# Kernel optimization log

Measured on AMD Instinct MI355X. Metric: run time of the kernel, lower is better.

## Reference

```python
import jax, jax.numpy as jnp
import numpy as np
import math

B, S, F_IN = 8, 1024, 32
D, H, L, NCLS = 512, 8, 6, 3
DFF = 4 * D
DK = D // H
EPS = 1e-5


def make_pe(max_len, d_model):
    pos = jnp.arange(max_len, dtype=jnp.float32)[:, None]
    div = jnp.exp(jnp.arange(0, d_model, 2, dtype=jnp.float32) * (-math.log(10000.0) / d_model))
    pe = jnp.zeros((max_len, d_model), dtype=jnp.float32)
    pe = pe.at[:, 0::2].set(jnp.sin(pos * div))
    pe = pe.at[:, 1::2].set(jnp.cos(pos * div))
    return pe  # [max_len, D]


def layernorm(x, g, b):
    m = jnp.mean(x, -1, keepdims=True)
    v = jnp.mean((x - m) ** 2, -1, keepdims=True)
    return (x - m) * jax.lax.rsqrt(v + EPS) * g + b


def setup_inputs() -> dict:
    key = jax.random.key(0)
    ks = iter(jax.random.split(key, 40))

    def w(shape, scale=None):
        k = next(ks)
        s = scale if scale is not None else 1.0 / math.sqrt(shape[0])
        return jax.random.normal(k, shape, dtype=jnp.float32) * s

    inp = {
        'x': jax.random.normal(next(ks), (B, S, F_IN), dtype=jnp.float32),
        'pe': make_pe(S, D),
        'emb_w': w((F_IN, D)), 'emb_b': jnp.zeros((D,), jnp.float32),
        'Wq': w((L, D, D)), 'bq': jnp.zeros((L, D), jnp.float32),
        'Wk': w((L, D, D)), 'bk': jnp.zeros((L, D), jnp.float32),
        'Wv': w((L, D, D)), 'bv': jnp.zeros((L, D), jnp.float32),
        'Wo': w((L, D, D)), 'bo': jnp.zeros((L, D), jnp.float32),
        'ln1_g': jnp.ones((L, D), jnp.float32), 'ln1_b': jnp.zeros((L, D), jnp.float32),
        'ln2_g': jnp.ones((L, D), jnp.float32), 'ln2_b': jnp.zeros((L, D), jnp.float32),
        'W1': w((L, D, DFF)), 'b1': jnp.zeros((L, DFF), jnp.float32),
        'W2': w((L, DFF, D)), 'b2': jnp.zeros((L, D), jnp.float32),
        'fc1_w': w((D, 256)), 'fc1_b': jnp.zeros((256,), jnp.float32),
        'fc2_w': w((256, 128)), 'fc2_b': jnp.zeros((128,), jnp.float32),
        'fc3_w': w((128, NCLS)), 'fc3_b': jnp.zeros((NCLS,), jnp.float32),
    }
    return inp


def reference(x, pe, emb_w, emb_b, Wq, bq, Wk, bk, Wv, bv, Wo, bo,
              ln1_g, ln1_b, ln2_g, ln2_b, W1, b1, W2, b2,
              fc1_w, fc1_b, fc2_w, fc2_b, fc3_w, fc3_b):
    scale = math.sqrt(DK)
    h = x @ emb_w + emb_b                      # [B,S,D]
    h = h + pe[None, :S, :]                    # positional encoding
    for l in range(L):
        # multi-head self-attention (full O(S^2) scores, as in source)
        q = (h @ Wq[l] + bq[l]).reshape(B, S, H, DK).transpose(0, 2, 1, 3)
        k = (h @ Wk[l] + bk[l]).reshape(B, S, H, DK).transpose(0, 2, 1, 3)
        v = (h @ Wv[l] + bv[l]).reshape(B, S, H, DK).transpose(0, 2, 1, 3)
        scores = jnp.einsum('bhqd,bhkd->bhqk', q, k) / scale   # [B,H,S,S]
        attn = jax.nn.softmax(scores, axis=-1)
        ctx = jnp.einsum('bhqk,bhkd->bhqd', attn, v)           # [B,H,S,DK]
        ctx = ctx.transpose(0, 2, 1, 3).reshape(B, S, D)
        attn_out = ctx @ Wo[l] + bo[l]
        h = layernorm(h + attn_out, ln1_g[l], ln1_b[l])
        ff = jax.nn.relu(h @ W1[l] + b1[l]) @ W2[l] + b2[l]
        h = layernorm(h + ff, ln2_g[l], ln2_b[l])
    pooled = jnp.mean(h, axis=1)               # AdaptiveAvgPool1d(1) over seq
    z = jax.nn.relu(pooled @ fc1_w + fc1_b)
    z = jax.nn.relu(z @ fc2_w + fc2_b)
    return z @ fc3_w + fc3_b                   # [B, NCLS]
```

## Files before the change

kernel.cpp:

```cpp
#include <hip/hip_runtime.h>
#include <math.h>

#define B_   8
#define S_   1024
#define FIN  32
#define D_   512
#define H_   8
#define L_   6
#define DFF_ 2048
#define DK_  64

__device__ __forceinline__ float mulrn(float a, float b) { return __fmul_rn(a, b); }
__device__ __forceinline__ float addrn(float a, float b) { return __fadd_rn(a, b); }

__global__ __launch_bounds__(128) void k_embed(const float* __restrict__ x,
                                               const float* __restrict__ emb_w,
                                               const float* __restrict__ emb_b,
                                               const float* __restrict__ pe,
                                               float* __restrict__ h) {
    int row = blockIdx.x;
    int s = row & (S_ - 1);
    int t = threadIdx.x;
    __shared__ float xs[FIN];
    if (t < FIN) xs[t] = x[row * FIN + t];
    __syncthreads();
    int d = t * 4;
    float a0 = 0.f, a1 = 0.f, a2 = 0.f, a3 = 0.f;
#pragma unroll
    for (int k = 0; k < FIN; ++k) {
        float xv = xs[k];
        const float* wr = &emb_w[k * D_ + d];
        a0 = fmaf(xv, wr[0], a0);
        a1 = fmaf(xv, wr[1], a1);
        a2 = fmaf(xv, wr[2], a2);
        a3 = fmaf(xv, wr[3], a3);
    }
    const float* bb = &emb_b[d];
    const float* pp = &pe[s * D_ + d];
    float4 o;
    o.x = addrn(addrn(a0, bb[0]), pp[0]);
    o.y = addrn(addrn(a1, bb[1]), pp[1]);
    o.z = addrn(addrn(a2, bb[2]), pp[2]);
    o.w = addrn(addrn(a3, bb[3]), pp[3]);
    *(float4*)&h[(size_t)row * D_ + d] = o;
}

template<bool RELU>
__global__ __launch_bounds__(256) void k_gemm(const float* __restrict__ A,
                                              const float* __restrict__ W,
                                              const float* __restrict__ bias,
                                              float* __restrict__ C,
                                              int M, int N, int K) {
    __shared__ float As[16][68];
    __shared__ float Bs[16][68];
    int bm = blockIdx.y * 64, bn = blockIdx.x * 64;
    int t = threadIdx.x;
    int tr = t >> 4, tc = t & 15;
    int ar = t >> 2, ak = (t & 3) * 4;
    int wk = t >> 4, wn = (t & 15) * 4;
    float acc[4][4] = {};
    for (int k0 = 0; k0 < K; k0 += 16) {
        float4 a4 = *(const float4*)&A[(size_t)(bm + ar) * K + k0 + ak];
        float4 w4 = *(const float4*)&W[(size_t)(k0 + wk) * N + bn + wn];
        __syncthreads();
        As[ak + 0][ar] = a4.x; As[ak + 1][ar] = a4.y;
        As[ak + 2][ar] = a4.z; As[ak + 3][ar] = a4.w;
        *(float4*)&Bs[wk][wn] = w4;
        __syncthreads();
#pragma unroll
        for (int kk = 0; kk < 16; ++kk) {
            float4 av = *(const float4*)&As[kk][tr * 4];
            float4 bv = *(const float4*)&Bs[kk][tc * 4];
            acc[0][0] = fmaf(av.x, bv.x, acc[0][0]); acc[0][1] = fmaf(av.x, bv.y, acc[0][1]);
            acc[0][2] = fmaf(av.x, bv.z, acc[0][2]); acc[0][3] = fmaf(av.x, bv.w, acc[0][3]);
            acc[1][0] = fmaf(av.y, bv.x, acc[1][0]); acc[1][1] = fmaf(av.y, bv.y, acc[1][1]);
            acc[1][2] = fmaf(av.y, bv.z, acc[1][2]); acc[1][3] = fmaf(av.y, bv.w, acc[1][3]);
            acc[2][0] = fmaf(av.z, bv.x, acc[2][0]); acc[2][1] = fmaf(av.z, bv.y, acc[2][1]);
            acc[2][2] = fmaf(av.z, bv.z, acc[2][2]); acc[2][3] = fmaf(av.z, bv.w, acc[2][3]);
            acc[3][0] = fmaf(av.w, bv.x, acc[3][0]); acc[3][1] = fmaf(av.w, bv.y, acc[3][1]);
            acc[3][2] = fmaf(av.w, bv.z, acc[3][2]); acc[3][3] = fmaf(av.w, bv.w, acc[3][3]);
        }
    }
    float4 b4 = *(const float4*)&bias[bn + tc * 4];
#pragma unroll
    for (int i = 0; i < 4; ++i) {
        float4 o;
        o.x = addrn(acc[i][0], b4.x); o.y = addrn(acc[i][1], b4.y);
        o.z = addrn(acc[i][2], b4.z); o.w = addrn(acc[i][3], b4.w);
        if (RELU) {
            o.x = fmaxf(o.x, 0.f); o.y = fmaxf(o.y, 0.f);
            o.z = fmaxf(o.z, 0.f); o.w = fmaxf(o.w, 0.f);
        }
        *(float4*)&C[(size_t)(bm + tr * 4 + i) * N + bn + tc * 4] = o;
    }
}

__global__ __launch_bounds__(256) void k_attn(const float* q,
                                              const float* __restrict__ kg,
                                              const float* __restrict__ vg,
                                              float* ctx) {
    __shared__ float KVs[32][68];
    __shared__ float Ss[16 * 1024];
    int hh = blockIdx.x;
    int ch = blockIdx.y;
    int b  = blockIdx.z;
    int t  = threadIdx.x;
    int r  = t >> 4, c16 = t & 15;
    const int row0 = ch * 16;
    const size_t base = (size_t)b * S_ * D_ + hh * DK_;


    {
        int rr = t >> 4, cc = (t & 15) * 4;
        *(float4*)&KVs[rr][cc] = *(const float4*)&q[base + (size_t)(row0 + rr) * D_ + cc];
    }
    __syncthreads();
    float4 qr[16];
#pragma unroll
    for (int i = 0; i < 16; ++i) qr[i] = *(float4*)&KVs[r][i * 4];

    for (int kt = 0; kt < 32; ++kt) {
        __syncthreads();
#pragma unroll
        for (int i = 0; i < 2; ++i) {
            int fid = t + i * 256;
            int rr = fid >> 4, cc = (fid & 15) * 4;
            *(float4*)&KVs[rr][cc] = *(const float4*)&kg[base + (size_t)(kt * 32 + rr) * D_ + cc];
        }
        __syncthreads();
        float s0 = 0.f, s1 = 0.f;
#pragma unroll
        for (int d4 = 0; d4 < 16; ++d4) {
            float4 qv = qr[d4];
            float4 k0 = *(float4*)&KVs[c16][d4 * 4];
            float4 k1 = *(float4*)&KVs[c16 + 16][d4 * 4];
            s0 = addrn(s0, mulrn(qv.x, k0.x)); s1 = addrn(s1, mulrn(qv.x, k1.x));
            s0 = addrn(s0, mulrn(qv.y, k0.y)); s1 = addrn(s1, mulrn(qv.y, k1.y));
            s0 = addrn(s0, mulrn(qv.z, k0.z)); s1 = addrn(s1, mulrn(qv.z, k1.z));
            s0 = addrn(s0, mulrn(qv.w, k0.w)); s1 = addrn(s1, mulrn(qv.w, k1.w));
        }
#pragma unroll
        for (int u = 0; u < 2; ++u) {
            int jglob = kt * 32 + u * 16 + c16;
            int sl = jglob >> 6, jj = jglob & 63;
            Ss[(r << 10) + (sl << 6) + ((jj + sl + (r << 3)) & 63)] =
                mulrn(u == 0 ? s0 : s1, 0.125f);
        }
    }
    __syncthreads();

    const int sbase = (r << 10) + (c16 << 6);
    const int rot   = c16 + (r << 3);
    float mx = -INFINITY;
    for (int j = 0; j < 64; ++j) mx = fmaxf(mx, Ss[sbase + ((j + rot) & 63)]);
    mx = fmaxf(mx, __shfl_xor(mx, 1));
    mx = fmaxf(mx, __shfl_xor(mx, 2));
    mx = fmaxf(mx, __shfl_xor(mx, 4));
    mx = fmaxf(mx, __shfl_xor(mx, 8));

    float psum = 0.f;
    for (int j = 0; j < 64; ++j) {
        int p_ = sbase + ((j + rot) & 63);
        float p = expf(__fsub_rn(Ss[p_], mx));
        Ss[p_] = p;
        psum = addrn(psum, p);
    }
    psum = addrn(psum, __shfl_xor(psum, 1));
    psum = addrn(psum, __shfl_xor(psum, 2));
    psum = addrn(psum, __shfl_xor(psum, 4));
    psum = addrn(psum, __shfl_xor(psum, 8));
    for (int j = 0; j < 64; ++j) {
        int p_ = sbase + ((j + rot) & 63);
        Ss[p_] = __fdiv_rn(Ss[p_], psum);
    }

    int d0 = c16 * 4;
    float a0 = 0.f, a1 = 0.f, a2 = 0.f, a3 = 0.f;
    for (int vt = 0; vt < 32; ++vt) {
        __syncthreads();
#pragma unroll
        for (int i = 0; i < 2; ++i) {
            int fid = t + i * 256;
            int rr = fid >> 4, cc = (fid & 15) * 4;
            *(float4*)&KVs[rr][cc] = *(const float4*)&vg[base + (size_t)(vt * 32 + rr) * D_ + cc];
        }
        __syncthreads();
#pragma unroll 8
        for (int jl = 0; jl < 32; ++jl) {
            int j = vt * 32 + jl;
            int sl = j >> 6;
            float p = Ss[(r << 10) + (sl << 6) + (((j & 63) + sl + (r << 3)) & 63)];
            float4 v4 = *(float4*)&KVs[jl][d0];
            a0 = addrn(a0, mulrn(p, v4.x));
            a1 = addrn(a1, mulrn(p, v4.y));
            a2 = addrn(a2, mulrn(p, v4.z));
            a3 = addrn(a3, mulrn(p, v4.w));
        }
    }
    float4 o = {a0, a1, a2, a3};
    *(float4*)&ctx[base + (size_t)(row0 + r) * D_ + d0] = o;
}

__global__ __launch_bounds__(256) void k_add_ln(float* h,
                                                const float* __restrict__ res,
                                                const float* __restrict__ g,
                                                const float* __restrict__ bta) {
    int row = blockIdx.x;
    int t = threadIdx.x;
    size_t base = (size_t)row * D_;
    float y0 = addrn(h[base + t],       res[base + t]);
    float y1 = addrn(h[base + t + 256], res[base + t + 256]);
    __shared__ float red[4];
    int w = t >> 6;
    float s = y0 + y1;
#pragma unroll
    for (int o = 1; o < 64; o <<= 1) s += __shfl_xor(s, o);
    if ((t & 63) == 0) red[w] = s;
    __syncthreads();
    float mean = (red[0] + red[1] + red[2] + red[3]) * (1.f / D_);
    __syncthreads();
    float d0 = __fsub_rn(y0, mean), d1 = __fsub_rn(y1, mean);
    s = mulrn(d0, d0) + mulrn(d1, d1);
#pragma unroll
    for (int o = 1; o < 64; o <<= 1) s += __shfl_xor(s, o);
    if ((t & 63) == 0) red[w] = s;
    __syncthreads();
    float var = (red[0] + red[1] + red[2] + red[3]) * (1.f / D_);
    float rstd = __fdiv_rn(1.0f, sqrtf(__fadd_rn(var, 1e-5f)));
    h[base + t]       = addrn(mulrn(mulrn(d0, rstd), g[t]),       bta[t]);
    h[base + t + 256] = addrn(mulrn(mulrn(d1, rstd), g[t + 256]), bta[t + 256]);
}

__global__ __launch_bounds__(256) void k_pool(const float* __restrict__ h,
                                              float* __restrict__ pooled) {
    int blk = blockIdx.x;
    int b = blk >> 3, dc = (blk & 7) * 64;
    int t = threadIdx.x;
    int d = dc + (t & 63), sg = t >> 6;
    float s = 0.f;
    for (int ss = sg; ss < S_; ss += 4)
        s = addrn(s, h[((size_t)b * S_ + ss) * D_ + d]);
    __shared__ float sh[4][64];
    sh[sg][t & 63] = s;
    __syncthreads();
    if (t < 64)
        pooled[b * D_ + dc + t] = (sh[0][t] + sh[1][t] + sh[2][t] + sh[3][t]) * (1.f / S_);
}

__global__ __launch_bounds__(256) void k_head(const float* __restrict__ pooled,
                                              const float* __restrict__ w1, const float* __restrict__ b1,
                                              const float* __restrict__ w2, const float* __restrict__ b2,
                                              const float* __restrict__ w3, const float* __restrict__ b3,
                                              float* __restrict__ out) {
    __shared__ float ps[B_][D_];
    __shared__ float z1[B_][256];
    __shared__ float z2[B_][128];
    int t = threadIdx.x;
    for (int i = t; i < B_ * D_; i += 256) ps[i >> 9][i & 511] = pooled[i];
    __syncthreads();
    {
        float acc[B_] = {};
        for (int k = 0; k < D_; ++k) {
            float w = w1[k * 256 + t];
#pragma unroll
            for (int b = 0; b < B_; ++b) acc[b] = fmaf(ps[b][k], w, acc[b]);
        }
#pragma unroll
        for (int b = 0; b < B_; ++b) z1[b][t] = fmaxf(addrn(acc[b], b1[t]), 0.f);
    }
    __syncthreads();
    if (t < 128) {
        float acc[B_] = {};
        for (int k = 0; k < 256; ++k) {
            float w = w2[k * 128 + t];
#pragma unroll
            for (int b = 0; b < B_; ++b) acc[b] = fmaf(z1[b][k], w, acc[b]);
        }
#pragma unroll
        for (int b = 0; b < B_; ++b) z2[b][t] = fmaxf(addrn(acc[b], b2[t]), 0.f);
    }
    __syncthreads();
    if (t < B_ * 3) {
        int b = t / 3, c = t % 3;
        float acc = 0.f;
        for (int k = 0; k < 128; ++k) acc = fmaf(z2[b][k], w3[k * 3 + c], acc);
        out[t] = addrn(acc, b3[c]);
    }
}

extern "C" void kernel_launch(void* const* d_in, const int* in_sizes, int n_in,
                              void* d_out, int out_size, void* d_ws, size_t ws_size,
                              hipStream_t stream) {
    const float* x     = (const float*)d_in[0];
    const float* pe    = (const float*)d_in[1];
    const float* emb_w = (const float*)d_in[2];
    const float* emb_b = (const float*)d_in[3];
    const float* Wq    = (const float*)d_in[4];
    const float* bq    = (const float*)d_in[5];
    const float* Wk    = (const float*)d_in[6];
    const float* bk    = (const float*)d_in[7];
    const float* Wv    = (const float*)d_in[8];
    const float* bv    = (const float*)d_in[9];
    const float* Wo    = (const float*)d_in[10];
    const float* bo    = (const float*)d_in[11];
    const float* ln1_g = (const float*)d_in[12];
    const float* ln1_b = (const float*)d_in[13];
    const float* ln2_g = (const float*)d_in[14];
    const float* ln2_b = (const float*)d_in[15];
    const float* W1    = (const float*)d_in[16];
    const float* b1    = (const float*)d_in[17];
    const float* W2    = (const float*)d_in[18];
    const float* b2    = (const float*)d_in[19];
    const float* fc1_w = (const float*)d_in[20];
    const float* fc1_b = (const float*)d_in[21];
    const float* fc2_w = (const float*)d_in[22];
    const float* fc2_b = (const float*)d_in[23];
    const float* fc3_w = (const float*)d_in[24];
    const float* fc3_b = (const float*)d_in[25];

    const size_t NBS = (size_t)B_ * S_ * D_;
    float* ws = (float*)d_ws;
    const int MROWS = B_ * S_;

    float* h = ws;
    float* q = h + NBS;
    float* k = q + NBS;
    float* v = k + NBS;
    float* pooled = v + NBS;

    k_embed<<<MROWS, 128, 0, stream>>>(x, emb_w, emb_b, pe, h);

    dim3 g512(D_ / 64, MROWS / 64);
    dim3 gff(DFF_ / 64, 4096 / 64);
    dim3 gw2(D_ / 64, 4096 / 64);
    dim3 gattn(H_, S_ / 16, B_);

    for (int l = 0; l < L_; ++l) {
        const float* wq = Wq + (size_t)l * D_ * D_;
        const float* wk = Wk + (size_t)l * D_ * D_;
        const float* wv = Wv + (size_t)l * D_ * D_;
        const float* wo = Wo + (size_t)l * D_ * D_;
        k_gemm<false><<<g512, 256, 0, stream>>>(h, wq, bq + l * D_, q, MROWS, D_, D_);
        k_gemm<false><<<g512, 256, 0, stream>>>(h, wk, bk + l * D_, k, MROWS, D_, D_);
        k_gemm<false><<<g512, 256, 0, stream>>>(h, wv, bv + l * D_, v, MROWS, D_, D_);
        k_attn<<<gattn, 256, 0, stream>>>(q, k, v, q);
        k_gemm<false><<<g512, 256, 0, stream>>>(q, wo, bo + l * D_, k, MROWS, D_, D_);
        k_add_ln<<<MROWS, 256, 0, stream>>>(h, k, ln1_g + l * D_, ln1_b + l * D_);
        for (int c = 0; c < 2; ++c) {
            float* ff1 = q;
            k_gemm<true ><<<gff, 256, 0, stream>>>(h + (size_t)c * 4096 * D_,
                W1 + (size_t)l * D_ * DFF_, b1 + l * DFF_, ff1, 4096, DFF_, D_);
            k_gemm<false><<<gw2, 256, 0, stream>>>(ff1,
                W2 + (size_t)l * DFF_ * D_, b2 + l * D_, v + (size_t)c * 4096 * D_, 4096, D_, DFF_);
        }
        k_add_ln<<<MROWS, 256, 0, stream>>>(h, v, ln2_g + l * D_, ln2_b + l * D_);
    }

    k_pool<<<B_ * 8, 256, 0, stream>>>(h, pooled);
    k_head<<<1, 256, 0, stream>>>(pooled, fc1_w, fc1_b, fc2_w, fc2_b, fc3_w, fc3_b, (float*)d_out);
}
```

Measured before the change: 8.590 ms.

## Enlarge GEMM register tiles and software-prefetch K/V tiles in attention

The FP32 GEMM is templated on the per-thread tile size. Projections and FF1 now use 8x8 outputs per thread (128x128 block tiles), and the W2 GEMM uses 4x8 (64x128). The aim is more FMA work per shared-memory load and fewer global loads per output. The attention kernel now loads the next K/V tile into registers while computing on the current one, overlapping global memory latency with compute. The cost is higher register pressure, which may reduce occupancy, and fewer blocks in the grids for these GEMMs.

Measured after the change: 9.849 ms. 14.7% more time.

```diff
diff --git a/kernel.cpp b/kernel.cpp
--- a/kernel.cpp
+++ b/kernel.cpp
@@ -45,53 +45,74 @@
     *(float4*)&h[(size_t)row * D_ + d] = o;
 }
 
-template<bool RELU>
+template<int TM, int TN, bool RELU>
 __global__ __launch_bounds__(256) void k_gemm(const float* __restrict__ A,
                                               const float* __restrict__ W,
                                               const float* __restrict__ bias,
                                               float* __restrict__ C,
                                               int M, int N, int K) {
-    __shared__ float As[16][68];
-    __shared__ float Bs[16][68];
-    int bm = blockIdx.y * 64, bn = blockIdx.x * 64;
+    constexpr int BM = 16 * TM, BN = 16 * TN;
+    constexpr int LA = TM / 4, LW = TN / 4;
+    __shared__ float As[16][BM + 4];
+    __shared__ float Bs[16][BN + 4];
+    int bm = blockIdx.y * BM, bn = blockIdx.x * BN;
     int t = threadIdx.x;
     int tr = t >> 4, tc = t & 15;
-    int ar = t >> 2, ak = (t & 3) * 4;
-    int wk = t >> 4, wn = (t & 15) * 4;
-    float acc[4][4] = {};
+    float acc[TM][TN] = {};
     for (int k0 = 0; k0 < K; k0 += 16) {
-        float4 a4 = *(const float4*)&A[(size_t)(bm + ar) * K + k0 + ak];
-        float4 w4 = *(const float4*)&W[(size_t)(k0 + wk) * N + bn + wn];
+        float4 pa[LA], pw[LW];
+#pragma unroll
+        for (int i = 0; i < LA; ++i) {
+            int fid = i * 256 + t;
+            pa[i] = *(const float4*)&A[(size_t)(bm + (fid >> 2)) * K + k0 + (fid & 3) * 4];
+        }
+#pragma unroll
+        for (int i = 0; i < LW; ++i) {
+            int fid = i * 256 + t;
+            pw[i] = *(const float4*)&W[(size_t)(k0 + fid / (BN / 4)) * N + bn + (fid % (BN / 4)) * 4];
+        }
         __syncthreads();
-        As[ak + 0][ar] = a4.x; As[ak + 1][ar] = a4.y;
-        As[ak + 2][ar] = a4.z; As[ak + 3][ar] = a4.w;
-        *(float4*)&Bs[wk][wn] = w4;
+#pragma unroll
+        for (int i = 0; i < LA; ++i) {
+            int fid = i * 256 + t, row = fid >> 2, kq = (fid & 3) * 4;
+            As[kq + 0][row] = pa[i].x; As[kq + 1][row] = pa[i].y;
+            As[kq + 2][row] = pa[i].z; As[kq + 3][row] = pa[i].w;
+        }
+#pragma unroll
+        for (int i = 0; i < LW; ++i) {
+            int fid = i * 256 + t;
+            *(float4*)&Bs[fid / (BN / 4)][(fid % (BN / 4)) * 4] = pw[i];
+        }
         __syncthreads();
 #pragma unroll
         for (int kk = 0; kk < 16; ++kk) {
-            float4 av = *(const float4*)&As[kk][tr * 4];
-            float4 bv = *(const float4*)&Bs[kk][tc * 4];
-            acc[0][0] = fmaf(av.x, bv.x, acc[0][0]); acc[0][1] = fmaf(av.x, bv.y, acc[0][1]);
-            acc[0][2] = fmaf(av.x, bv.z, acc[0][2]); acc[0][3] = fmaf(av.x, bv.w, acc[0][3]);
-            acc[1][0] = fmaf(av.y, bv.x, acc[1][0]); acc[1][1] = fmaf(av.y, bv.y, acc[1][1]);
-            acc[1][2] = fmaf(av.y, bv.z, acc[1][2]); acc[1][3] = fmaf(av.y, bv.w, acc[1][3]);
-            acc[2][0] = fmaf(av.z, bv.x, acc[2][0]); acc[2][1] = fmaf(av.z, bv.y, acc[2][1]);
-            acc[2][2] = fmaf(av.z, bv.z, acc[2][2]); acc[2][3] = fmaf(av.z, bv.w, acc[2][3]);
-            acc[3][0] = fmaf(av.w, bv.x, acc[3][0]); acc[3][1] = fmaf(av.w, bv.y, acc[3][1]);
-            acc[3][2] = fmaf(av.w, bv.z, acc[3][2]); acc[3][3] = fmaf(av.w, bv.w, acc[3][3]);
-        }
-    }
-    float4 b4 = *(const float4*)&bias[bn + tc * 4];
-#pragma unroll
-    for (int i = 0; i < 4; ++i) {
-        float4 o;
-        o.x = addrn(acc[i][0], b4.x); o.y = addrn(acc[i][1], b4.y);
-        o.z = addrn(acc[i][2], b4.z); o.w = addrn(acc[i][3], b4.w);
-        if (RELU) {
-            o.x = fmaxf(o.x, 0.f); o.y = fmaxf(o.y, 0.f);
-            o.z = fmaxf(o.z, 0.f); o.w = fmaxf(o.w, 0.f);
-        }
-        *(float4*)&C[(size_t)(bm + tr * 4 + i) * N + bn + tc * 4] = o;
+            float a[TM], b[TN];
+#pragma unroll
+            for (int i = 0; i < TM; i += 4) *(float4*)&a[i] = *(float4*)&As[kk][tr * TM + i];
+#pragma unroll
+            for (int j = 0; j < TN; j += 4) *(float4*)&b[j] = *(float4*)&Bs[kk][tc * TN + j];
+#pragma unroll
+            for (int i = 0; i < TM; ++i)
+#pragma unroll
+                for (int j = 0; j < TN; ++j)
+                    acc[i][j] = fmaf(a[i], b[j], acc[i][j]);
+        }
+    }
+#pragma unroll
+    for (int i = 0; i < TM; ++i) {
+#pragma unroll
+        for (int j = 0; j < TN; j += 4) {
+            float4 o;
+            o.x = addrn(acc[i][j + 0], bias[bn + tc * TN + j + 0]);
+            o.y = addrn(acc[i][j + 1], bias[bn + tc * TN + j + 1]);
+            o.z = addrn(acc[i][j + 2], bias[bn + tc * TN + j + 2]);
+            o.w = addrn(acc[i][j + 3], bias[bn + tc * TN + j + 3]);
+            if (RELU) {
+                o.x = fmaxf(o.x, 0.f); o.y = fmaxf(o.y, 0.f);
+                o.z = fmaxf(o.z, 0.f); o.w = fmaxf(o.w, 0.f);
+            }
+            *(float4*)&C[(size_t)(bm + tr * TM + i) * N + bn + tc * TN + j] = o;
+        }
     }
 }
 
@@ -108,26 +129,26 @@
     int r  = t >> 4, c16 = t & 15;
     const int row0 = ch * 16;
     const size_t base = (size_t)b * S_ * D_ + hh * DK_;
-
-
-    {
-        int rr = t >> 4, cc = (t & 15) * 4;
-        *(float4*)&KVs[rr][cc] = *(const float4*)&q[base + (size_t)(row0 + rr) * D_ + cc];
-    }
+    const int srr = t >> 4, scc = (t & 15) * 4;
+
+    *(float4*)&KVs[srr][scc] = *(const float4*)&q[base + (size_t)(row0 + srr) * D_ + scc];
     __syncthreads();
     float4 qr[16];
 #pragma unroll
     for (int i = 0; i < 16; ++i) qr[i] = *(float4*)&KVs[r][i * 4];
 
+    float4 nx0 = *(const float4*)&kg[base + (size_t)srr * D_ + scc];
+    float4 nx1 = *(const float4*)&kg[base + (size_t)(srr + 16) * D_ + scc];
+    __syncthreads();
+    *(float4*)&KVs[srr][scc] = nx0;
+    *(float4*)&KVs[srr + 16][scc] = nx1;
+    __syncthreads();
     for (int kt = 0; kt < 32; ++kt) {
-        __syncthreads();
-#pragma unroll
-        for (int i = 0; i < 2; ++i) {
-            int fid = t + i * 256;
-            int rr = fid >> 4, cc = (fid & 15) * 4;
-            *(float4*)&KVs[rr][cc] = *(const float4*)&kg[base + (size_t)(kt * 32 + rr) * D_ + cc];
-        }
-        __syncthreads();
+        if (kt < 31) {
+            size_t rowb = base + (size_t)((kt + 1) * 32) * D_;
+            nx0 = *(const float4*)&kg[rowb + (size_t)srr * D_ + scc];
+            nx1 = *(const float4*)&kg[rowb + (size_t)(srr + 16) * D_ + scc];
+        }
         float s0 = 0.f, s1 = 0.f;
 #pragma unroll
         for (int d4 = 0; d4 < 16; ++d4) {
@@ -146,8 +167,13 @@
             Ss[(r << 10) + (sl << 6) + ((jj + sl + (r << 3)) & 63)] =
                 mulrn(u == 0 ? s0 : s1, 0.125f);
         }
-    }
-    __syncthreads();
+        __syncthreads();
+        if (kt < 31) {
+            *(float4*)&KVs[srr][scc] = nx0;
+            *(float4*)&KVs[srr + 16][scc] = nx1;
+            __syncthreads();
+        }
+    }
 
     const int sbase = (r << 10) + (c16 << 6);
     const int rot   = c16 + (r << 3);
@@ -176,15 +202,18 @@
 
     int d0 = c16 * 4;
     float a0 = 0.f, a1 = 0.f, a2 = 0.f, a3 = 0.f;
+    nx0 = *(const float4*)&vg[base + (size_t)srr * D_ + scc];
+    nx1 = *(const float4*)&vg[base + (size_t)(srr + 16) * D_ + scc];
+    __syncthreads();
+    *(float4*)&KVs[srr][scc] = nx0;
+    *(float4*)&KVs[srr + 16][scc] = nx1;
+    __syncthreads();
     for (int vt = 0; vt < 32; ++vt) {
-        __syncthreads();
-#pragma unroll
-        for (int i = 0; i < 2; ++i) {
-            int fid = t + i * 256;
-            int rr = fid >> 4, cc = (fid & 15) * 4;
-            *(float4*)&KVs[rr][cc] = *(const float4*)&vg[base + (size_t)(vt * 32 + rr) * D_ + cc];
-        }
-        __syncthreads();
+        if (vt < 31) {
+            size_t rowb = base + (size_t)((vt + 1) * 32) * D_;
+            nx0 = *(const float4*)&vg[rowb + (size_t)srr * D_ + scc];
+            nx1 = *(const float4*)&vg[rowb + (size_t)(srr + 16) * D_ + scc];
+        }
 #pragma unroll 8
         for (int jl = 0; jl < 32; ++jl) {
             int j = vt * 32 + jl;
@@ -195,6 +224,12 @@
             a1 = addrn(a1, mulrn(p, v4.y));
             a2 = addrn(a2, mulrn(p, v4.z));
             a3 = addrn(a3, mulrn(p, v4.w));
+        }
+        __syncthreads();
+        if (vt < 31) {
+            *(float4*)&KVs[srr][scc] = nx0;
+            *(float4*)&KVs[srr + 16][scc] = nx1;
+            __syncthreads();
         }
     }
     float4 o = {a0, a1, a2, a3};
@@ -330,9 +365,9 @@
 
     k_embed<<<MROWS, 128, 0, stream>>>(x, emb_w, emb_b, pe, h);
 
-    dim3 g512(D_ / 64, MROWS / 64);
-    dim3 gff(DFF_ / 64, 4096 / 64);
-    dim3 gw2(D_ / 64, 4096 / 64);
+    dim3 g512(D_ / 128, MROWS / 128);
+    dim3 gff(DFF_ / 128, 4096 / 128);
+    dim3 gw2(D_ / 128, 4096 / 64);
     dim3 gattn(H_, S_ / 16, B_);
 
     for (int l = 0; l < L_; ++l) {
@@ -340,17 +375,17 @@
         const float* wk = Wk + (size_t)l * D_ * D_;
         const float* wv = Wv + (size_t)l * D_ * D_;
         const float* wo = Wo + (size_t)l * D_ * D_;
-        k_gemm<false><<<g512, 256, 0, stream>>>(h, wq, bq + l * D_, q, MROWS, D_, D_);
-        k_gemm<false><<<g512, 256, 0, stream>>>(h, wk, bk + l * D_, k, MROWS, D_, D_);
-        k_gemm<false><<<g512, 256, 0, stream>>>(h, wv, bv + l * D_, v, MROWS, D_, D_);
+        k_gemm<8, 8, false><<<g512, 256, 0, stream>>>(h, wq, bq + l * D_, q, MROWS, D_, D_);
+        k_gemm<8, 8, false><<<g512, 256, 0, stream>>>(h, wk, bk + l * D_, k, MROWS, D_, D_);
+        k_gemm<8, 8, false><<<g512, 256, 0, stream>>>(h, wv, bv + l * D_, v, MROWS, D_, D_);
         k_attn<<<gattn, 256, 0, stream>>>(q, k, v, q);
-        k_gemm<false><<<g512, 256, 0, stream>>>(q, wo, bo + l * D_, k, MROWS, D_, D_);
+        k_gemm<8, 8, false><<<g512, 256, 0, stream>>>(q, wo, bo + l * D_, k, MROWS, D_, D_);
         k_add_ln<<<MROWS, 256, 0, stream>>>(h, k, ln1_g + l * D_, ln1_b + l * D_);
         for (int c = 0; c < 2; ++c) {
             float* ff1 = q;
-            k_gemm<true ><<<gff, 256, 0, stream>>>(h + (size_t)c * 4096 * D_,
+            k_gemm<8, 8, true ><<<gff, 256, 0, stream>>>(h + (size_t)c * 4096 * D_,
                 W1 + (size_t)l * D_ * DFF_, b1 + l * DFF_, ff1, 4096, DFF_, D_);
-            k_gemm<false><<<gw2, 256, 0, stream>>>(ff1,
+            k_gemm<4, 8, false><<<gw2, 256, 0, stream>>>(ff1,
                 W2 + (size_t)l * DFF_ * D_, b2 + l * D_, v + (size_t)c * 4096 * D_, 4096, D_, DFF_);
         }
         k_add_ln<<<MROWS, 256, 0, stream>>>(h, v, ln2_g + l * D_, ln2_b + l * D_);
```

## Prefetch next tiles into registers in GEMM and attention loops

Applied to the files above, without the earlier changes.

The GEMM kernel now double-buffers its shared-memory tiles and loads the next K-slice into registers while computing on the current one, which removes one barrier per iteration. The attention kernel likewise prefetches the next K and V tiles into registers during compute, and replaces the modular index arithmetic in the softmax and PV loops with incremental offsets. The aim is to hide global-load latency behind FMAs. In exchange it raises register pressure and doubles GEMM LDS use, which could lower occupancy.

Measured after the change: 7.914 ms. 1.09x faster.

```diff
diff --git a/kernel.cpp b/kernel.cpp
--- a/kernel.cpp
+++ b/kernel.cpp
@@ -51,26 +51,33 @@
                                               const float* __restrict__ bias,
                                               float* __restrict__ C,
                                               int M, int N, int K) {
-    __shared__ float As[16][68];
-    __shared__ float Bs[16][68];
+    __shared__ float As[2][16][68];
+    __shared__ float Bs[2][16][68];
     int bm = blockIdx.y * 64, bn = blockIdx.x * 64;
     int t = threadIdx.x;
     int tr = t >> 4, tc = t & 15;
     int ar = t >> 2, ak = (t & 3) * 4;
     int wk = t >> 4, wn = (t & 15) * 4;
     float acc[4][4] = {};
-    for (int k0 = 0; k0 < K; k0 += 16) {
-        float4 a4 = *(const float4*)&A[(size_t)(bm + ar) * K + k0 + ak];
-        float4 w4 = *(const float4*)&W[(size_t)(k0 + wk) * N + bn + wn];
-        __syncthreads();
-        As[ak + 0][ar] = a4.x; As[ak + 1][ar] = a4.y;
-        As[ak + 2][ar] = a4.z; As[ak + 3][ar] = a4.w;
-        *(float4*)&Bs[wk][wn] = w4;
-        __syncthreads();
+
+    float4 pa = *(const float4*)&A[(size_t)(bm + ar) * K + ak];
+    float4 pw = *(const float4*)&W[(size_t)wk * N + bn + wn];
+    As[0][ak + 0][ar] = pa.x; As[0][ak + 1][ar] = pa.y;
+    As[0][ak + 2][ar] = pa.z; As[0][ak + 3][ar] = pa.w;
+    *(float4*)&Bs[0][wk][wn] = pw;
+    __syncthreads();
+
+    const int nP = K >> 4;
+    for (int p = 0; p < nP; ++p) {
+        int cur = p & 1;
+        if (p + 1 < nP) {
+            pa = *(const float4*)&A[(size_t)(bm + ar) * K + (p + 1) * 16 + ak];
+            pw = *(const float4*)&W[(size_t)((p + 1) * 16 + wk) * N + bn + wn];
+        }
 #pragma unroll
         for (int kk = 0; kk < 16; ++kk) {
-            float4 av = *(const float4*)&As[kk][tr * 4];
-            float4 bv = *(const float4*)&Bs[kk][tc * 4];
+            float4 av = *(const float4*)&As[cur][kk][tr * 4];
+            float4 bv = *(const float4*)&Bs[cur][kk][tc * 4];
             acc[0][0] = fmaf(av.x, bv.x, acc[0][0]); acc[0][1] = fmaf(av.x, bv.y, acc[0][1]);
             acc[0][2] = fmaf(av.x, bv.z, acc[0][2]); acc[0][3] = fmaf(av.x, bv.w, acc[0][3]);
             acc[1][0] = fmaf(av.y, bv.x, acc[1][0]); acc[1][1] = fmaf(av.y, bv.y, acc[1][1]);
@@ -80,6 +87,13 @@
             acc[3][0] = fmaf(av.w, bv.x, acc[3][0]); acc[3][1] = fmaf(av.w, bv.y, acc[3][1]);
             acc[3][2] = fmaf(av.w, bv.z, acc[3][2]); acc[3][3] = fmaf(av.w, bv.w, acc[3][3]);
         }
+        if (p + 1 < nP) {
+            int nxt = cur ^ 1;
+            As[nxt][ak + 0][ar] = pa.x; As[nxt][ak + 1][ar] = pa.y;
+            As[nxt][ak + 2][ar] = pa.z; As[nxt][ak + 3][ar] = pa.w;
+            *(float4*)&Bs[nxt][wk][wn] = pw;
+        }
+        __syncthreads();
     }
     float4 b4 = *(const float4*)&bias[bn + tc * 4];
 #pragma unroll
@@ -108,26 +122,26 @@
     int r  = t >> 4, c16 = t & 15;
     const int row0 = ch * 16;
     const size_t base = (size_t)b * S_ * D_ + hh * DK_;
-
-
-    {
-        int rr = t >> 4, cc = (t & 15) * 4;
-        *(float4*)&KVs[rr][cc] = *(const float4*)&q[base + (size_t)(row0 + rr) * D_ + cc];
-    }
+    const int srr = t >> 4, scc = (t & 15) * 4;
+
+    *(float4*)&KVs[srr][scc] = *(const float4*)&q[base + (size_t)(row0 + srr) * D_ + scc];
     __syncthreads();
     float4 qr[16];
 #pragma unroll
     for (int i = 0; i < 16; ++i) qr[i] = *(float4*)&KVs[r][i * 4];
 
+    float4 nx0 = *(const float4*)&kg[base + (size_t)srr * D_ + scc];
+    float4 nx1 = *(const float4*)&kg[base + (size_t)(srr + 16) * D_ + scc];
+    __syncthreads();
+    *(float4*)&KVs[srr][scc] = nx0;
+    *(float4*)&KVs[srr + 16][scc] = nx1;
+    __syncthreads();
     for (int kt = 0; kt < 32; ++kt) {
-        __syncthreads();
-#pragma unroll
-        for (int i = 0; i < 2; ++i) {
-            int fid = t + i * 256;
-            int rr = fid >> 4, cc = (fid & 15) * 4;
-            *(float4*)&KVs[rr][cc] = *(const float4*)&kg[base + (size_t)(kt * 32 + rr) * D_ + cc];
-        }
-        __syncthreads();
+        if (kt < 31) {
+            size_t rowb = base + (size_t)((kt + 1) * 32) * D_;
+            nx0 = *(const float4*)&kg[rowb + (size_t)srr * D_ + scc];
+            nx1 = *(const float4*)&kg[rowb + (size_t)(srr + 16) * D_ + scc];
+        }
         float s0 = 0.f, s1 = 0.f;
 #pragma unroll
         for (int d4 = 0; d4 < 16; ++d4) {
@@ -146,55 +160,85 @@
             Ss[(r << 10) + (sl << 6) + ((jj + sl + (r << 3)) & 63)] =
                 mulrn(u == 0 ? s0 : s1, 0.125f);
         }
-    }
-    __syncthreads();
+        __syncthreads();
+        if (kt < 31) {
+            *(float4*)&KVs[srr][scc] = nx0;
+            *(float4*)&KVs[srr + 16][scc] = nx1;
+            __syncthreads();
+        }
+    }
 
     const int sbase = (r << 10) + (c16 << 6);
-    const int rot   = c16 + (r << 3);
+    const int rot   = (c16 + (r << 3)) & 63;
     float mx = -INFINITY;
-    for (int j = 0; j < 64; ++j) mx = fmaxf(mx, Ss[sbase + ((j + rot) & 63)]);
+    {
+        int off = rot;
+        for (int j = 0; j < 64; ++j) {
+            mx = fmaxf(mx, Ss[sbase + off]);
+            off = (off + 1) & 63;
+        }
+    }
     mx = fmaxf(mx, __shfl_xor(mx, 1));
     mx = fmaxf(mx, __shfl_xor(mx, 2));
     mx = fmaxf(mx, __shfl_xor(mx, 4));
     mx = fmaxf(mx, __shfl_xor(mx, 8));
 
     float psum = 0.f;
-    for (int j = 0; j < 64; ++j) {
-        int p_ = sbase + ((j + rot) & 63);
-        float p = expf(__fsub_rn(Ss[p_], mx));
-        Ss[p_] = p;
-        psum = addrn(psum, p);
+    {
+        int off = rot;
+        for (int j = 0; j < 64; ++j) {
+            int p_ = sbase + off;
+            float p = expf(__fsub_rn(Ss[p_], mx));
+            Ss[p_] = p;
+            psum = addrn(psum, p);
+            off = (off + 1) & 63;
+        }
     }
     psum = addrn(psum, __shfl_xor(psum, 1));
     psum = addrn(psum, __shfl_xor(psum, 2));
     psum = addrn(psum, __shfl_xor(psum, 4));
     psum = addrn(psum, __shfl_xor(psum, 8));
-    for (int j = 0; j < 64; ++j) {
-        int p_ = sbase + ((j + rot) & 63);
-        Ss[p_] = __fdiv_rn(Ss[p_], psum);
+    {
+        int off = rot;
+        for (int j = 0; j < 64; ++j) {
+            int p_ = sbase + off;
+            Ss[p_] = __fdiv_rn(Ss[p_], psum);
+            off = (off + 1) & 63;
+        }
     }
 
     int d0 = c16 * 4;
     float a0 = 0.f, a1 = 0.f, a2 = 0.f, a3 = 0.f;
+    nx0 = *(const float4*)&vg[base + (size_t)srr * D_ + scc];
+    nx1 = *(const float4*)&vg[base + (size_t)(srr + 16) * D_ + scc];
+    __syncthreads();
+    *(float4*)&KVs[srr][scc] = nx0;
+    *(float4*)&KVs[srr + 16][scc] = nx1;
+    __syncthreads();
     for (int vt = 0; vt < 32; ++vt) {
-        __syncthreads();
-#pragma unroll
-        for (int i = 0; i < 2; ++i) {
-            int fid = t + i * 256;
-            int rr = fid >> 4, cc = (fid & 15) * 4;
-            *(float4*)&KVs[rr][cc] = *(const float4*)&vg[base + (size_t)(vt * 32 + rr) * D_ + cc];
-        }
-        __syncthreads();
+        if (vt < 31) {
+            size_t rowb = base + (size_t)((vt + 1) * 32) * D_;
+            nx0 = *(const float4*)&vg[rowb + (size_t)srr * D_ + scc];
+            nx1 = *(const float4*)&vg[rowb + (size_t)(srr + 16) * D_ + scc];
+        }
+        int sl = vt >> 1;
+        const float* srow = &Ss[(r << 10) + (sl << 6)];
+        int off = (((vt & 1) << 5) + sl + (r << 3)) & 63;
 #pragma unroll 8
         for (int jl = 0; jl < 32; ++jl) {
-            int j = vt * 32 + jl;
-            int sl = j >> 6;
-            float p = Ss[(r << 10) + (sl << 6) + (((j & 63) + sl + (r << 3)) & 63)];
+            float p = srow[off];
+            off = (off + 1) & 63;
             float4 v4 = *(float4*)&KVs[jl][d0];
             a0 = addrn(a0, mulrn(p, v4.x));
             a1 = addrn(a1, mulrn(p, v4.y));
             a2 = addrn(a2, mulrn(p, v4.z));
             a3 = addrn(a3, mulrn(p, v4.w));
+        }
+        __syncthreads();
+        if (vt < 31) {
+            *(float4*)&KVs[srr][scc] = nx0;
+            *(float4*)&KVs[srr + 16][scc] = nx1;
+            __syncthreads();
         }
     }
     float4 o = {a0, a1, a2, a3};
```
